# Optimization experiments

Hardware: AMD Instinct MI355X
Metric: run time of the kernel (lower is better)

## Reference

```python
import jax, jax.numpy as jnp
import numpy as np

B, N, D = 2, 2048, 1024
H, HD = 16, 64


def setup_inputs() -> dict:
    key = jax.random.key(0)
    ks = jax.random.split(key, 5)
    return {
        "hidden_states": jax.random.normal(ks[0], (B, N, D), dtype=jnp.float32),
        "W_attn": jax.random.normal(ks[1], (D, 3 * D), dtype=jnp.float32) * (D ** -0.5),
        "b_attn": jax.random.normal(ks[2], (3 * D,), dtype=jnp.float32) * 0.02,
        "W_proj": jax.random.normal(ks[3], (D, D), dtype=jnp.float32) * (D ** -0.5),
        "b_proj": jax.random.normal(ks[4], (D,), dtype=jnp.float32) * 0.02,
    }


def reference(hidden_states, W_attn, b_attn, W_proj, b_proj):
    # QKV projection: [B,N,3D]
    proj = hidden_states @ W_attn + b_attn
    q, k, v = jnp.split(proj, 3, axis=-1)
    # [B,N,H,HD]
    q = q.reshape(B, N, H, HD)
    k = k.reshape(B, N, H, HD)
    v = v.reshape(B, N, H, HD)
    scale = HD ** -0.5
    # naive attention: full [B,H,Nq,Nkv] score matrix
    attn = jnp.einsum("bqhd,bkhd->bhqk", q, k) * scale
    q_pos = jnp.arange(N)
    kv_pos = jnp.arange(N)
    # mask where kv_pos > start_pos + q_pos (start_pos = 0)
    mask = kv_pos[None, :] > q_pos[:, None]  # [Nq, Nkv]
    attn = jnp.where(mask[None, None, :, :], -jnp.inf, attn)
    attn = jax.nn.softmax(attn, axis=-1)
    out = jnp.einsum("bhqk,bkhd->bqhd", attn, v)  # [B,N,H,HD]
    out = out.reshape(B, N, D)
    return out @ W_proj + b_proj
```

## Files before the change

### kernel.cpp

```cpp
#include <hip/hip_runtime.h>
#include <hip/hip_bf16.h>

#define BB 2
#define NN 2048
#define DDIM 1024
#define HH 16
#define HDD 64

typedef __attribute__((ext_vector_type(8))) short bf16x8;
typedef __attribute__((ext_vector_type(4))) short bf16x4;
typedef __attribute__((ext_vector_type(4))) float f32x4;

__device__ inline ushort f2bf(float x) {
  __hip_bfloat16 h = __float2bfloat16(x);
  ushort u;
  __builtin_memcpy(&u, &h, 2);
  return u;
}
__device__ inline float bf2f(ushort u) {
  unsigned v = (unsigned)u << 16;
  float f;
  __builtin_memcpy(&f, &v, 4);
  return f;
}
__device__ inline float exp2_raw(float x) {
  float r;
  asm("v_exp_f32 %0, %1" : "=v"(r) : "v"(x));
  return r;
}

#define GLOAD_LDS16(g, l)                                                              \
  __builtin_amdgcn_global_load_lds((const __attribute__((address_space(1))) void*)(g), \
                                   (__attribute__((address_space(3))) void*)(l), 16, 0, 0)

__global__ __launch_bounds__(256) void cvt_f32_bf16(const float* __restrict__ in,
                                                    ushort* __restrict__ out, int n4) {
  int i = blockIdx.x * 256 + threadIdx.x;
  if (i >= n4) return;
  float4 a = ((const float4*)in)[i];
  ushort4 o;
  o.x = f2bf(a.x); o.y = f2bf(a.y); o.z = f2bf(a.z); o.w = f2bf(a.w);
  ((ushort4*)out)[i] = o;
}

__global__ __launch_bounds__(256) void transpose_cvt(const float* __restrict__ in,
                                                     ushort* __restrict__ out, int R, int C) {
  __shared__ float tile[32][33];
  int bx = blockIdx.x * 32, by = blockIdx.y * 32;
  int tx = threadIdx.x, ty = threadIdx.y;
#pragma unroll
  for (int r = ty; r < 32; r += 8)
    tile[r][tx] = in[(size_t)(by + r) * C + bx + tx];
  __syncthreads();
#pragma unroll
  for (int r = ty; r < 32; r += 8)
    out[(size_t)(bx + r) * R + by + tx] = f2bf(tile[tx][r]);
}

template <int MODE>
__global__ __launch_bounds__(256) void gemm_bt(const ushort* __restrict__ A,
                                               const ushort* __restrict__ Bt,
                                               const float* __restrict__ bias,
                                               void* __restrict__ Cv,
                                               ushort* __restrict__ Vt,
                                               int M, int N, int K) {
  __shared__ ushort As[128 * 32];
  __shared__ ushort Bs[128 * 32];
  const int tid = threadIdx.x;
  const int wid = tid >> 6, lane = tid & 63;
  const int c = lane & 15, g = lane >> 4;
  const int wm = (wid >> 1) * 64, wn = (wid & 1) * 64;
  const int m0 = blockIdx.y * 128, n0 = blockIdx.x * 128;
  f32x4 acc[4][4] = {};
  for (int k0 = 0; k0 < K; k0 += 32) {
    __syncthreads();
#pragma unroll
    for (int it = 0; it < 2; ++it) {
      int G = tid + it * 256;
      int row = G >> 2, sl = G & 3;
      GLOAD_LDS16(A + (size_t)(m0 + row) * K + k0 + sl * 8, &As[G * 8]);
      GLOAD_LDS16(Bt + (size_t)(n0 + row) * K + k0 + sl * 8, &Bs[G * 8]);
    }
    __syncthreads();
    bf16x8 af[4], bfr[4];
#pragma unroll
    for (int i = 0; i < 4; ++i) {
      af[i] = *(const bf16x8*)(&As[(wm + i * 16 + c) * 32 + g * 8]);
      bfr[i] = *(const bf16x8*)(&Bs[(wn + i * 16 + c) * 32 + g * 8]);
    }
#pragma unroll
    for (int i = 0; i < 4; ++i)
#pragma unroll
      for (int j = 0; j < 4; ++j)
        acc[i][j] = __builtin_amdgcn_mfma_f32_16x16x32_bf16(af[i], bfr[j], acc[i][j], 0, 0, 0);
  }
#pragma unroll
  for (int i = 0; i < 4; ++i) {
#pragma unroll
    for (int j = 0; j < 4; ++j) {
      const int col = n0 + wn + j * 16 + c;
      const float bv = bias[col];
      const int row = m0 + wm + i * 16 + g * 4;
      if (MODE == 2 && col >= 2048) {
        const int hh = (col - 2048) >> 6, dd = (col - 2048) & 63;
        const int bb = row >> 11, nl = row & 2047;
        ushort4 ov;
        ov.x = f2bf(acc[i][j][0] + bv);
        ov.y = f2bf(acc[i][j][1] + bv);
        ov.z = f2bf(acc[i][j][2] + bv);
        ov.w = f2bf(acc[i][j][3] + bv);
        *(ushort4*)(&Vt[(size_t)((bb * 16 + hh) * 64 + dd) * NN + nl]) = ov;
      } else {
        const int ldc = (MODE == 2) ? 2048 : N;
#pragma unroll
        for (int ri = 0; ri < 4; ++ri) {
          float v = acc[i][j][ri] + bv;
          ((ushort*)Cv)[(size_t)(row + ri) * ldc + col] = f2bf(v);
        }
      }
    }
  }
}

__global__ __launch_bounds__(256) void gemm_proj(const ushort* __restrict__ A,
                                                 const ushort* __restrict__ Bt,
                                                 const float* __restrict__ bias,
                                                 float* __restrict__ C, int M, int N, int K) {
  __shared__ ushort As[64 * 32];
  __shared__ ushort Bs[128 * 32];
  const int tid = threadIdx.x;
  const int wid = tid >> 6, lane = tid & 63;
  const int c = lane & 15, g = lane >> 4;
  const int wn = wid * 32;
  const int m0 = blockIdx.y * 64, n0 = blockIdx.x * 128;
  f32x4 acc[4][2] = {};
  for (int k0 = 0; k0 < K; k0 += 32) {
    __syncthreads();
#pragma unroll
    for (int it = 0; it < 3; ++it) {
      int G = tid + it * 256;
      if (G < 256) {
        int row = G >> 2, sl = G & 3;
        GLOAD_LDS16(A + (size_t)(m0 + row) * K + k0 + sl * 8, &As[G * 8]);
      } else {
        int GB = G - 256;
        int row = GB >> 2, sl = GB & 3;
        GLOAD_LDS16(Bt + (size_t)(n0 + row) * K + k0 + sl * 8, &Bs[GB * 8]);
      }
    }
    __syncthreads();
    bf16x8 af[4], bfr[2];
#pragma unroll
    for (int i = 0; i < 4; ++i) af[i] = *(const bf16x8*)(&As[(i * 16 + c) * 32 + g * 8]);
#pragma unroll
    for (int j = 0; j < 2; ++j)
      bfr[j] = *(const bf16x8*)(&Bs[(wn + j * 16 + c) * 32 + g * 8]);
#pragma unroll
    for (int i = 0; i < 4; ++i)
#pragma unroll
      for (int j = 0; j < 2; ++j)
        acc[i][j] = __builtin_amdgcn_mfma_f32_16x16x32_bf16(af[i], bfr[j], acc[i][j], 0, 0, 0);
  }
#pragma unroll
  for (int i = 0; i < 4; ++i) {
#pragma unroll
    for (int j = 0; j < 2; ++j) {
      const int col = n0 + wn + j * 16 + c;
      const float bv = bias[col];
      const int row = m0 + i * 16 + g * 4;
#pragma unroll
      for (int ri = 0; ri < 4; ++ri)
        C[(size_t)(row + ri) * N + col] = acc[i][j][ri] + bv;
    }
  }
}

__global__ __launch_bounds__(256) void attn_fwd(const ushort* __restrict__ QK,
                                                const ushort* __restrict__ Vt,
                                                ushort* __restrict__ O) {
  const int bh = blockIdx.x;
  const int b = bh >> 4, h = bh & 15;
  const int qb = (int)gridDim.y - 1 - (int)blockIdx.y;
  const int tid = threadIdx.x;
  const int wid = tid >> 6, lane = tid & 63;
  const int c = lane & 15, g = lane >> 4;
  const int q0 = qb * 64 + wid * 16;
  const ushort* Qb = QK + (size_t)b * NN * 2048 + (size_t)h * HDD;
  const ushort* Kb = Qb + 1024;
  const ushort* Vb = Vt + (size_t)bh * HDD * NN;

  __shared__ ushort Ks[2][64 * 64];
  __shared__ ushort Vs[2][64 * 64];

  const float SC = 0.18033688011112042f;
  bf16x8 qf[2];
  {
    const ushort* qrow = Qb + (size_t)(q0 + c) * 2048 + g * 8;
    qf[0] = *(const bf16x8*)(qrow);
    qf[1] = *(const bf16x8*)(qrow + 32);
#pragma unroll
    for (int r = 0; r < 2; ++r)
#pragma unroll
      for (int e = 0; e < 8; ++e) qf[r][e] = (short)f2bf(bf2f((ushort)qf[r][e]) * SC);
  }

  f32x4 oacc[4] = {};
  float m = 0.f, lsum = 0.f;
  const int q_abs = q0 + c;

#define STAGE_TILE(kv0, bufi)                                                   \
  do {                                                                          \
    _Pragma("unroll") for (int it = 0; it < 2; ++it) {                          \
      int u = tid + it * 256;                                                   \
      int row = u >> 3, sl = u & 7;                                             \
      int ksl = (sl ^ (row & 7)) * 8;                                           \
      GLOAD_LDS16(Kb + (size_t)((kv0) + row) * 2048 + ksl, &Ks[bufi][u * 8]);   \
      GLOAD_LDS16(Vb + (size_t)row * NN + (kv0) + ksl, &Vs[bufi][u * 8]);       \
    }                                                                           \
  } while (0)

  STAGE_TILE(0, 0);
  __syncthreads();
  int cur = 0;

  for (int t = 0; t <= qb; ++t) {
    if (t < qb) STAGE_TILE((t + 1) * 64, cur ^ 1);

    f32x4 s[4] = {};
#pragma unroll
    for (int f = 0; f < 4; ++f) {
      int krow = f * 16 + c;
#pragma unroll
      for (int dc = 0; dc < 2; ++dc) {
        int slot = (dc * 4 + g) ^ (krow & 7);
        bf16x8 kf = *(const bf16x8*)(&Ks[cur][krow * 64 + slot * 8]);
        s[f] = __builtin_amdgcn_mfma_f32_16x16x32_bf16(kf, qf[dc], s[f], 0, 0, 0);
      }
    }

    float pmax = -INFINITY;
    if (t == qb) {
      const int kv0 = t * 64;
#pragma unroll
      for (int f = 0; f < 4; ++f)
#pragma unroll
        for (int i = 0; i < 4; ++i) {
          if (kv0 + f * 16 + g * 4 + i > q_abs) s[f][i] = -INFINITY;
          pmax = fmaxf(pmax, s[f][i]);
        }
    } else {
#pragma unroll
      for (int f = 0; f < 4; ++f)
#pragma unroll
        for (int i = 0; i < 4; ++i) pmax = fmaxf(pmax, s[f][i]);
    }

    if (t == 0) {
      float pr = fmaxf(pmax, __shfl_xor(pmax, 16));
      pr = fmaxf(pr, __shfl_xor(pr, 32));
      m = pr;
    } else if (!__all(pmax <= m + 8.f)) {
      float pr = fmaxf(pmax, __shfl_xor(pmax, 16));
      pr = fmaxf(pr, __shfl_xor(pr, 32));
      float mnew = fmaxf(m, pr);
      float corr = exp2_raw(m - mnew);
      lsum *= corr;
#pragma unroll
      for (int db = 0; db < 4; ++db) {
        oacc[db][0] *= corr; oacc[db][1] *= corr;
        oacc[db][2] *= corr; oacc[db][3] *= corr;
      }
      m = mnew;
    }

    float psum = 0.f;
#pragma unroll
    for (int f = 0; f < 4; ++f)
#pragma unroll
      for (int i = 0; i < 4; ++i) {
        float p = exp2_raw(s[f][i] - m);
        s[f][i] = p;
        psum += p;
      }
    lsum += psum;

#pragma unroll
    for (int f = 0; f < 4; ++f) {
      bf16x4 pb;
      pb[0] = (short)f2bf(s[f][0]);
      pb[1] = (short)f2bf(s[f][1]);
      pb[2] = (short)f2bf(s[f][2]);
      pb[3] = (short)f2bf(s[f][3]);
      const int slot = f * 2 + (g >> 1);
#pragma unroll
      for (int db = 0; db < 4; ++db) {
        int d = db * 16 + c;
        bf16x4 vf =
            *(const bf16x4*)(&Vs[cur][d * 64 + ((slot ^ (d & 7)) * 8) + (g & 1) * 4]);
        oacc[db] = __builtin_amdgcn_mfma_f32_16x16x16bf16_1k(vf, pb, oacc[db], 0, 0, 0);
      }
    }
    __syncthreads();
    cur ^= 1;
  }

  lsum += __shfl_xor(lsum, 16);
  lsum += __shfl_xor(lsum, 32);
  float invl = 1.f / lsum;
  ushort* orow = O + (size_t)(b * NN + q0 + c) * DDIM + h * HDD;
#pragma unroll
  for (int db = 0; db < 4; ++db) {
    ushort4 ov;
    ov.x = f2bf(oacc[db][0] * invl);
    ov.y = f2bf(oacc[db][1] * invl);
    ov.z = f2bf(oacc[db][2] * invl);
    ov.w = f2bf(oacc[db][3] * invl);
    *(ushort4*)(&orow[db * 16 + g * 4]) = ov;
  }
}

extern "C" void kernel_launch(void* const* d_in, const int* in_sizes, int n_in,
                              void* d_out, int out_size, void* d_ws, size_t ws_size,
                              hipStream_t stream) {
  const float* hidden = (const float*)d_in[0];
  const float* W_attn = (const float*)d_in[1];
  const float* b_attn = (const float*)d_in[2];
  const float* W_proj = (const float*)d_in[3];
  const float* b_proj = (const float*)d_in[4];

  char* ws = (char*)d_ws;
  ushort* hbf  = (ushort*)(ws);
  ushort* WaT  = (ushort*)(ws + (size_t)(8 << 20));
  ushort* WpT  = (ushort*)(ws + (size_t)(14 << 20));
  ushort* qk   = (ushort*)(ws + (size_t)(16 << 20));
  ushort* vt   = (ushort*)(ws + (size_t)(32 << 20));
  ushort* aout = (ushort*)(ws + (size_t)(40 << 20));

  cvt_f32_bf16<<<4096, 256, 0, stream>>>(hidden, hbf, (BB * NN * DDIM) / 4);
  transpose_cvt<<<dim3(96, 32), dim3(32, 8), 0, stream>>>(W_attn, WaT, 1024, 3072);
  transpose_cvt<<<dim3(32, 32), dim3(32, 8), 0, stream>>>(W_proj, WpT, 1024, 1024);

  gemm_bt<2><<<dim3(24, 32), 256, 0, stream>>>(hbf, WaT, b_attn, qk, vt, 4096, 3072, 1024);
  attn_fwd<<<dim3(32, 32), 256, 0, stream>>>(qk, vt, aout);
  gemm_proj<<<dim3(8, 64), 256, 0, stream>>>(aout, WpT, b_proj, (float*)d_out, 4096, 1024, 1024);
}
```

Measured before the change: 191.0 us.

## Process two 64-row query blocks per attention workgroup to reuse K/V tiles

Each attention workgroup now handles 128 query rows, as two 64-row sub-blocks held in registers per wave. Every staged K/V tile in LDS is therefore reused by twice as many queries, and the grid is halved. The first sub-block skips its MFMAs on the final tile, where it is fully masked. The cost is roughly double the accumulator and score registers per thread, which lowers occupancy, and fewer workgroups with more uneven causal work between them.

```diff
diff --git a/kernel.cpp b/kernel.cpp
--- a/kernel.cpp
+++ b/kernel.cpp
@@ -184,7 +184,7 @@
   const int tid = threadIdx.x;
   const int wid = tid >> 6, lane = tid & 63;
   const int c = lane & 15, g = lane >> 4;
-  const int q0 = qb * 64 + wid * 16;
+  const int q0 = qb * 128 + wid * 16;
   const ushort* Qb = QK + (size_t)b * NN * 2048 + (size_t)h * HDD;
   const ushort* Kb = Qb + 1024;
   const ushort* Vb = Vt + (size_t)bh * HDD * NN;
@@ -193,20 +193,22 @@
   __shared__ ushort Vs[2][64 * 64];
 
   const float SC = 0.18033688011112042f;
-  bf16x8 qf[2];
-  {
-    const ushort* qrow = Qb + (size_t)(q0 + c) * 2048 + g * 8;
-    qf[0] = *(const bf16x8*)(qrow);
-    qf[1] = *(const bf16x8*)(qrow + 32);
+  bf16x8 qf[2][2];
+#pragma unroll
+  for (int qr = 0; qr < 2; ++qr) {
+    const ushort* qrow = Qb + (size_t)(q0 + qr * 64 + c) * 2048 + g * 8;
+    qf[qr][0] = *(const bf16x8*)(qrow);
+    qf[qr][1] = *(const bf16x8*)(qrow + 32);
 #pragma unroll
     for (int r = 0; r < 2; ++r)
 #pragma unroll
-      for (int e = 0; e < 8; ++e) qf[r][e] = (short)f2bf(bf2f((ushort)qf[r][e]) * SC);
-  }
-
-  f32x4 oacc[4] = {};
-  float m = 0.f, lsum = 0.f;
-  const int q_abs = q0 + c;
+      for (int e = 0; e < 8; ++e)
+        qf[qr][r][e] = (short)f2bf(bf2f((ushort)qf[qr][r][e]) * SC);
+  }
+
+  f32x4 oacc[2][4] = {};
+  float m[2] = {0.f, 0.f}, lsum[2] = {0.f, 0.f};
+  const int q_abs[2] = {q0 + c, q0 + 64 + c};
 
 #define STAGE_TILE(kv0, bufi)                                                   \
   do {                                                                          \
@@ -222,11 +224,13 @@
   STAGE_TILE(0, 0);
   __syncthreads();
   int cur = 0;
-
-  for (int t = 0; t <= qb; ++t) {
-    if (t < qb) STAGE_TILE((t + 1) * 64, cur ^ 1);
-
-    f32x4 s[4] = {};
+  const int ntiles = 2 * qb + 2;
+
+  for (int t = 0; t < ntiles; ++t) {
+    if (t < ntiles - 1) STAGE_TILE((t + 1) * 64, cur ^ 1);
+    const bool act0 = (t <= 2 * qb);
+
+    f32x4 s[2][4] = {};
 #pragma unroll
     for (int f = 0; f < 4; ++f) {
       int krow = f * 16 + c;
@@ -234,88 +238,98 @@
       for (int dc = 0; dc < 2; ++dc) {
         int slot = (dc * 4 + g) ^ (krow & 7);
         bf16x8 kf = *(const bf16x8*)(&Ks[cur][krow * 64 + slot * 8]);
-        s[f] = __builtin_amdgcn_mfma_f32_16x16x32_bf16(kf, qf[dc], s[f], 0, 0, 0);
-      }
-    }
-
-    float pmax = -INFINITY;
-    if (t == qb) {
-      const int kv0 = t * 64;
-#pragma unroll
-      for (int f = 0; f < 4; ++f)
+        if (act0) s[0][f] = __builtin_amdgcn_mfma_f32_16x16x32_bf16(kf, qf[0][dc], s[0][f], 0, 0, 0);
+        s[1][f] = __builtin_amdgcn_mfma_f32_16x16x32_bf16(kf, qf[1][dc], s[1][f], 0, 0, 0);
+      }
+    }
+
+    bf16x4 pb[2][4];
+#pragma unroll
+    for (int qr = 0; qr < 2; ++qr) {
+      if (qr == 0 && !act0) continue;
+      float pmax = -INFINITY;
+      if (t == 2 * qb + qr) {
+        const int kv0 = t * 64;
+#pragma unroll
+        for (int f = 0; f < 4; ++f)
+#pragma unroll
+          for (int i = 0; i < 4; ++i) {
+            if (kv0 + f * 16 + g * 4 + i > q_abs[qr]) s[qr][f][i] = -INFINITY;
+            pmax = fmaxf(pmax, s[qr][f][i]);
+          }
+      } else {
+#pragma unroll
+        for (int f = 0; f < 4; ++f)
+#pragma unroll
+          for (int i = 0; i < 4; ++i) pmax = fmaxf(pmax, s[qr][f][i]);
+      }
+      if (t == 0) {
+        float pr = fmaxf(pmax, __shfl_xor(pmax, 16));
+        pr = fmaxf(pr, __shfl_xor(pr, 32));
+        m[qr] = pr;
+      } else if (!__all(pmax <= m[qr] + 8.f)) {
+        float pr = fmaxf(pmax, __shfl_xor(pmax, 16));
+        pr = fmaxf(pr, __shfl_xor(pr, 32));
+        float mnew = fmaxf(m[qr], pr);
+        float corr = exp2_raw(m[qr] - mnew);
+        lsum[qr] *= corr;
+#pragma unroll
+        for (int db = 0; db < 4; ++db) {
+          oacc[qr][db][0] *= corr; oacc[qr][db][1] *= corr;
+          oacc[qr][db][2] *= corr; oacc[qr][db][3] *= corr;
+        }
+        m[qr] = mnew;
+      }
+      float psum = 0.f;
+#pragma unroll
+      for (int f = 0; f < 4; ++f) {
 #pragma unroll
         for (int i = 0; i < 4; ++i) {
-          if (kv0 + f * 16 + g * 4 + i > q_abs) s[f][i] = -INFINITY;
-          pmax = fmaxf(pmax, s[f][i]);
+          float p = exp2_raw(s[qr][f][i] - m[qr]);
+          s[qr][f][i] = p;
+          psum += p;
         }
-    } else {
-#pragma unroll
-      for (int f = 0; f < 4; ++f)
-#pragma unroll
-        for (int i = 0; i < 4; ++i) pmax = fmaxf(pmax, s[f][i]);
-    }
-
-    if (t == 0) {
-      float pr = fmaxf(pmax, __shfl_xor(pmax, 16));
-      pr = fmaxf(pr, __shfl_xor(pr, 32));
-      m = pr;
-    } else if (!__all(pmax <= m + 8.f)) {
-      float pr = fmaxf(pmax, __shfl_xor(pmax, 16));
-      pr = fmaxf(pr, __shfl_xor(pr, 32));
-      float mnew = fmaxf(m, pr);
-      float corr = exp2_raw(m - mnew);
-      lsum *= corr;
-#pragma unroll
-      for (int db = 0; db < 4; ++db) {
-        oacc[db][0] *= corr; oacc[db][1] *= corr;
-        oacc[db][2] *= corr; oacc[db][3] *= corr;
-      }
-      m = mnew;
-    }
-
-    float psum = 0.f;
-#pragma unroll
-    for (int f = 0; f < 4; ++f)
-#pragma unroll
-      for (int i = 0; i < 4; ++i) {
-        float p = exp2_raw(s[f][i] - m);
-        s[f][i] = p;
-        psum += p;
-      }
-    lsum += psum;
+        pb[qr][f][0] = (short)f2bf(s[qr][f][0]);
+        pb[qr][f][1] = (short)f2bf(s[qr][f][1]);
+        pb[qr][f][2] = (short)f2bf(s[qr][f][2]);
+        pb[qr][f][3] = (short)f2bf(s[qr][f][3]);
+      }
+      lsum[qr] += psum;
+    }
 
 #pragma unroll
     for (int f = 0; f < 4; ++f) {
-      bf16x4 pb;
-      pb[0] = (short)f2bf(s[f][0]);
-      pb[1] = (short)f2bf(s[f][1]);
-      pb[2] = (short)f2bf(s[f][2]);
-      pb[3] = (short)f2bf(s[f][3]);
       const int slot = f * 2 + (g >> 1);
 #pragma unroll
       for (int db = 0; db < 4; ++db) {
         int d = db * 16 + c;
         bf16x4 vf =
             *(const bf16x4*)(&Vs[cur][d * 64 + ((slot ^ (d & 7)) * 8) + (g & 1) * 4]);
-        oacc[db] = __builtin_amdgcn_mfma_f32_16x16x16bf16_1k(vf, pb, oacc[db], 0, 0, 0);
+        if (act0)
+          oacc[0][db] = __builtin_amdgcn_mfma_f32_16x16x16bf16_1k(vf, pb[0][f], oacc[0][db], 0, 0, 0);
+        oacc[1][db] = __builtin_amdgcn_mfma_f32_16x16x16bf16_1k(vf, pb[1][f], oacc[1][db], 0, 0, 0);
       }
     }
     __syncthreads();
     cur ^= 1;
   }
 
-  lsum += __shfl_xor(lsum, 16);
-  lsum += __shfl_xor(lsum, 32);
-  float invl = 1.f / lsum;
-  ushort* orow = O + (size_t)(b * NN + q0 + c) * DDIM + h * HDD;
-#pragma unroll
-  for (int db = 0; db < 4; ++db) {
-    ushort4 ov;
-    ov.x = f2bf(oacc[db][0] * invl);
-    ov.y = f2bf(oacc[db][1] * invl);
-    ov.z = f2bf(oacc[db][2] * invl);
-    ov.w = f2bf(oacc[db][3] * invl);
-    *(ushort4*)(&orow[db * 16 + g * 4]) = ov;
+#pragma unroll
+  for (int qr = 0; qr < 2; ++qr) {
+    float l = lsum[qr];
+    l += __shfl_xor(l, 16);
+    l += __shfl_xor(l, 32);
+    float invl = 1.f / l;
+    ushort* orow = O + (size_t)(b * NN + q0 + qr * 64 + c) * DDIM + h * HDD;
+#pragma unroll
+    for (int db = 0; db < 4; ++db) {
+      ushort4 ov;
+      ov.x = f2bf(oacc[qr][db][0] * invl);
+      ov.y = f2bf(oacc[qr][db][1] * invl);
+      ov.z = f2bf(oacc[qr][db][2] * invl);
+      ov.w = f2bf(oacc[qr][db][3] * invl);
+      *(ushort4*)(&orow[db * 16 + g * 4]) = ov;
+    }
   }
 }
 
@@ -341,6 +355,6 @@
   transpose_cvt<<<dim3(32, 32), dim3(32, 8), 0, stream>>>(W_proj, WpT, 1024, 1024);
 
   gemm_bt<2><<<dim3(24, 32), 256, 0, stream>>>(hbf, WaT, b_attn, qk, vt, 4096, 3072, 1024);
-  attn_fwd<<<dim3(32, 32), 256, 0, stream>>>(qk, vt, aout);
+  attn_fwd<<<dim3(32, 16), 256, 0, stream>>>(qk, vt, aout);
   gemm_proj<<<dim3(8, 64), 256, 0, stream>>>(aout, WpT, b_proj, (float*)d_out, 4096, 1024, 1024);
 }
```

Result: slower. 210.3 us (+10.1%).
